# Optimization experiments

Hardware: AMD Instinct MI355X
Metric: run time of the kernel (lower is better)

Reference implementation:

```python
import jax, jax.numpy as jnp
import numpy as np

N = 25600            # 64 graphs x 400 ROIs
F_IN = 400
H = 128
E = 512000           # 8000 edges per graph
B = 64
G = 8
OUT = 2
NPG = 400            # nodes per graph
EPG = E // B         # edges per graph
BN_EPS = 1e-5


def _xavier(k, shape):
    lim = float(np.sqrt(6.0 / (shape[0] + shape[1])))
    return jax.random.uniform(k, shape, jnp.float32, -lim, lim)


def setup_inputs() -> dict:
    key = jax.random.key(0)
    ks = jax.random.split(key, 16)
    inp = {}
    inp["x"] = jax.random.normal(ks[0], (N, F_IN), jnp.float32)
    # within-graph random edges: local index + graph offset
    src_l = jax.random.randint(ks[1], (E,), 0, NPG, jnp.int32)
    dst_l = jax.random.randint(ks[2], (E,), 0, NPG, jnp.int32)
    off = (jnp.arange(E, dtype=jnp.int32) // EPG) * NPG
    inp["edge_index"] = jnp.stack([src_l + off, dst_l + off])
    inp["batch"] = (jnp.arange(N, dtype=jnp.int32) // NPG)
    inp["group_ids"] = jax.random.randint(ks[3], (N,), 0, G, jnp.int32)
    inp["ge"] = _xavier(ks[4], (G, 2))
    inp["he"] = _xavier(ks[5], (2, 2))
    dims = [(F_IN + 4, H), (H, H), (H, H)]
    for i, (di, do) in enumerate(dims):
        k1, k2 = jax.random.split(ks[6 + i])
        inp[f"w{i}a"] = _xavier(k1, (di, do))
        inp[f"b{i}a"] = jnp.zeros((do,), jnp.float32)
        inp[f"g{i}"] = jnp.ones((do,), jnp.float32)
        inp[f"be{i}"] = jnp.zeros((do,), jnp.float32)
        inp[f"w{i}b"] = _xavier(k2, (do, do))
        inp[f"b{i}b"] = jnp.zeros((do,), jnp.float32)
    inp["wfa"] = _xavier(ks[10], (H, H))
    inp["bfa"] = jnp.zeros((H,), jnp.float32)
    inp["wfb"] = _xavier(ks[11], (H, OUT))
    inp["bfb"] = jnp.zeros((OUT,), jnp.float32)
    return inp


def _bn(h, gamma, beta):
    # BatchNorm1d in training mode: stats over node dimension
    mu = jnp.mean(h, axis=0, keepdims=True)
    var = jnp.var(h, axis=0, keepdims=True)
    return gamma * (h - mu) * jax.lax.rsqrt(var + BN_EPS) + beta


def reference(x, edge_index, batch, group_ids, ge, he,
              w0a, b0a, g0, be0, w0b, b0b,
              w1a, b1a, g1, be1, w1b, b1b,
              w2a, b2a, g2, be2, w2b, b2b,
              wfa, bfa, wfb, bfb):
    n = x.shape[0]
    hemi = jnp.arange(n) % 2                      # [1::2] = 1
    h = jnp.concatenate([x, ge[group_ids], he[hemi]], axis=-1)  # [N, F_IN+4]
    src, dst = edge_index[0], edge_index[1]
    layers = [(w0a, b0a, g0, be0, w0b, b0b),
              (w1a, b1a, g1, be1, w1b, b1b),
              (w2a, b2a, g2, be2, w2b, b2b)]
    for wa, ba, g, be, wb, bb in layers:
        # GINConv (eps=0): x_i + sum_{(j,i)} x_j, then 2-layer MLP w/ batchnorm
        agg = jax.ops.segment_sum(h[src], dst, num_segments=N)
        z = h + agg
        z = jax.nn.relu(_bn(z @ wa + ba, g, be))  # dropout = identity (eval)
        h = jax.nn.relu(z @ wb + bb)              # outer ReLU from forward()
    pooled = jax.ops.segment_sum(h, batch, num_segments=B)  # global_add_pool
    return jax.nn.relu(pooled @ wfa + bfa) @ wfb + bfb
```

## Files before the change

kernel.cpp:

```cpp
#include <hip/hip_runtime.h>

#define N_NODES 25600
#define F_IN 400
#define NE 512000
#define NB 64
#define NPG 400
#define EPG 8000
#define BN_EPS 1e-5f

#define S_ROWS 448
#define S_COLS 448
#define S_COLS2 (S_COLS / 2)
#define AGG_TILES 7
#define SB_RPB 112
#define K0PAD 448

typedef __attribute__((ext_vector_type(8))) short short8;
typedef __attribute__((ext_vector_type(4))) short short4_t;
typedef __attribute__((ext_vector_type(4))) float floatx4;

__device__ __forceinline__ unsigned short f2bf(float f) {
    unsigned int u = __float_as_uint(f);
    u += 0x7FFF + ((u >> 16) & 1);
    return (unsigned short)(u >> 16);
}
__device__ __forceinline__ float bf2f(unsigned short s) {
    return __uint_as_float((unsigned int)s << 16);
}
__device__ __forceinline__ short u8bf(unsigned v) {
    return (short)(__float_as_uint((float)v) >> 16);
}


__global__ __launch_bounds__(256) void prep(const int* __restrict__ src,
                                            const int* __restrict__ dst,
                                            unsigned char* __restrict__ Sb,
                                            const float* __restrict__ wa0, const float* __restrict__ wa1,
                                            const float* __restrict__ wa2, const float* __restrict__ wb0,
                                            const float* __restrict__ wb1, const float* __restrict__ wb2,
                                            unsigned short* __restrict__ t0, unsigned short* __restrict__ t1,
                                            unsigned short* __restrict__ t2, unsigned short* __restrict__ t3,
                                            unsigned short* __restrict__ t4, unsigned short* __restrict__ t5,
                                            float* __restrict__ pstat) {
    __shared__ int cnt32[SB_RPB * NPG / 4];
    int tid = threadIdx.x;
    if (blockIdx.x < 256) {
        int b = blockIdx.x;
        int g = b >> 2, part = b & 3;
        int r0 = part * SB_RPB;
        for (int i = tid; i < SB_RPB * NPG / 4; i += 256) cnt32[i] = 0;
        __syncthreads();
        int ebase = g * EPG, nbase = g * NPG;
        for (int e = tid; e < EPG; e += 256) {
            int d = dst[ebase + e] - nbase;
            int dr = d - r0;
            if ((unsigned)dr < (unsigned)SB_RPB) {
                int s = src[ebase + e] - nbase;
                int idx = dr * NPG + s;
                atomicAdd(&cnt32[idx >> 2], (int)(1u << ((idx & 3) * 8)));
            }
        }
        __syncthreads();
        const unsigned char* cb = (const unsigned char*)cnt32;
        for (int i = tid; i < SB_RPB * (S_COLS / 8); i += 256) {
            int rr = i / (S_COLS / 8), c8 = (i % (S_COLS / 8)) * 8;
            int R = r0 + rr;
            unsigned pk = 0;
#pragma unroll
            for (int j = 0; j < 8; ++j) {
                int c = c8 + j;
                unsigned v = 0;
                if (R < NPG && c < NPG) v = (unsigned)cb[rr * NPG + c] + (c == R ? 1u : 0u);
                pk |= (v & 15u) << (4 * j);
            }
            *(unsigned*)&Sb[((size_t)g * S_ROWS + R) * S_COLS2 + (c8 >> 1)] = pk;
        }
        return;
    }
    int idx = (blockIdx.x - 256) * 256 + tid;
    if (idx < 3 * 2048 + 8192) pstat[idx] = 0.f;
    if (idx < 128 * K0PAD) {
        int n = idx / K0PAD, k = idx - n * K0PAD;
        t0[idx] = (k < 400) ? f2bf(wa0[(size_t)k * 128 + n]) : (unsigned short)0;
        return;
    }
    idx -= 128 * K0PAD;
    if (idx >= 5 * 128 * 128) return;
    int seg = idx >> 14;
    int r = idx & 16383;
    int n = r >> 7, k = r & 127;
    const float* srcs[5] = {wb0, wa1, wb1, wa2, wb2};
    unsigned short* dsts[5] = {t3, t1, t4, t2, t5};
    dsts[seg][r] = f2bf(srcs[seg][(size_t)k * 128 + n]);
}


__global__ __launch_bounds__(256) void gemm_embed64(const float* __restrict__ A,
                                                    const unsigned short* __restrict__ Wt,
                                                    const float* __restrict__ Wfull,
                                                    const int* __restrict__ gid,
                                                    const float* __restrict__ ge,
                                                    const float* __restrict__ he,
                                                    unsigned short* __restrict__ CtT) {
    __shared__ __align__(16) unsigned short As[64][72];
    __shared__ __align__(16) unsigned short Bs[128][72];
    __shared__ float Wex[4][128];
    int tid = threadIdx.x;
    int m0 = blockIdx.x * 64;
    int wave = tid >> 6, lane = tid & 63;
    int wcol = wave * 32;
    int fm = lane & 15, quad = lane >> 4;

    for (int i = tid; i < 512; i += 256)
        Wex[i >> 7][i & 127] = Wfull[(size_t)(400 + (i >> 7)) * 128 + (i & 127)];

    floatx4 acc[4][2];
#pragma unroll
    for (int rt = 0; rt < 4; ++rt)
#pragma unroll
        for (int ct = 0; ct < 2; ++ct) acc[rt][ct] = (floatx4){0.f, 0.f, 0.f, 0.f};

    const int rA = tid >> 2, kcA = (tid & 3) * 16;
    const int nB = tid >> 1, kcB = (tid & 1) * 32;
    float4 aP0, aP1, aP2, aP3;
    short8 bP0, bP1, bP2, bP3;

    auto loadK = [&](int ks) {
        int k0 = ks * 64;
        int kg = k0 + kcA;
        const float* ar = A + (size_t)(m0 + rA) * F_IN;
        if (kg + 15 < 400) {
            aP0 = *(const float4*)(ar + kg);
            aP1 = *(const float4*)(ar + kg + 4);
            aP2 = *(const float4*)(ar + kg + 8);
            aP3 = *(const float4*)(ar + kg + 12);
        } else {
            float v[16];
#pragma unroll
            for (int j = 0; j < 16; ++j) v[j] = (kg + j < 400) ? ar[kg + j] : 0.f;
            aP0 = (float4){v[0], v[1], v[2], v[3]};
            aP1 = (float4){v[4], v[5], v[6], v[7]};
            aP2 = (float4){v[8], v[9], v[10], v[11]};
            aP3 = (float4){v[12], v[13], v[14], v[15]};
        }
        const unsigned short* wr = Wt + (size_t)nB * K0PAD + k0 + kcB;
        bP0 = *(const short8*)wr;
        bP1 = *(const short8*)(wr + 8);
        bP2 = *(const short8*)(wr + 16);
        bP3 = *(const short8*)(wr + 24);
    };

    loadK(0);
    for (int ks = 0; ks < 7; ++ks) {
        {
            short8 s0, s1;
            s0[0] = (short)f2bf(aP0.x); s0[1] = (short)f2bf(aP0.y);
            s0[2] = (short)f2bf(aP0.z); s0[3] = (short)f2bf(aP0.w);
            s0[4] = (short)f2bf(aP1.x); s0[5] = (short)f2bf(aP1.y);
            s0[6] = (short)f2bf(aP1.z); s0[7] = (short)f2bf(aP1.w);
            s1[0] = (short)f2bf(aP2.x); s1[1] = (short)f2bf(aP2.y);
            s1[2] = (short)f2bf(aP2.z); s1[3] = (short)f2bf(aP2.w);
            s1[4] = (short)f2bf(aP3.x); s1[5] = (short)f2bf(aP3.y);
            s1[6] = (short)f2bf(aP3.z); s1[7] = (short)f2bf(aP3.w);
            *(short8*)&As[rA][kcA] = s0;
            *(short8*)&As[rA][kcA + 8] = s1;
            *(short8*)&Bs[nB][kcB] = bP0;
            *(short8*)&Bs[nB][kcB + 8] = bP1;
            *(short8*)&Bs[nB][kcB + 16] = bP2;
            *(short8*)&Bs[nB][kcB + 24] = bP3;
        }
        __syncthreads();
        if (ks + 1 < 7) loadK(ks + 1);
#pragma unroll
        for (int k0l = 0; k0l < 64; k0l += 32) {
            short8 af[4], bf[2];
#pragma unroll
            for (int rt = 0; rt < 4; ++rt)
                af[rt] = *(const short8*)&As[rt * 16 + fm][k0l + quad * 8];
#pragma unroll
            for (int ct = 0; ct < 2; ++ct)
                bf[ct] = *(const short8*)&Bs[wcol + ct * 16 + fm][k0l + quad * 8];
#pragma unroll
            for (int rt = 0; rt < 4; ++rt)
#pragma unroll
                for (int ct = 0; ct < 2; ++ct)
                    acc[rt][ct] = __builtin_amdgcn_mfma_f32_16x16x32_bf16(
                        af[rt], bf[ct], acc[rt][ct], 0, 0, 0);
        }
        __syncthreads();
    }

#pragma unroll
    for (int rt = 0; rt < 4; ++rt) {
#pragma unroll
        for (int ct = 0; ct < 2; ++ct) {
            int col = wcol + ct * 16 + fm;
            int row0 = m0 + rt * 16 + quad * 4;
            ushort4 o;
#pragma unroll
            for (int r = 0; r < 4; ++r) {
                int row = row0 + r;
                int gv = gid[row];
                float v = acc[rt][ct][r]
                        + ge[gv * 2] * Wex[0][col] + ge[gv * 2 + 1] * Wex[1][col]
                        + he[(row & 1) * 2] * Wex[2][col] + he[(row & 1) * 2 + 1] * Wex[3][col];
                ((unsigned short*)&o)[r] = f2bf(v);
            }
            *(ushort4*)&CtT[(size_t)col * N_NODES + row0] = o;
        }
    }
}


__global__ __launch_bounds__(256) void agg_mfma(const unsigned char* __restrict__ Sb,
                                                const unsigned short* __restrict__ tT,
                                                const float* __restrict__ bias,
                                                unsigned short* __restrict__ z,
                                                float* __restrict__ psumG,
                                                float* __restrict__ psqG) {
    __shared__ __align__(16) unsigned short As[64][72];
    __shared__ __align__(16) unsigned short Bs[128][72];
    __shared__ float sw[4][2][16], qw[4][2][16];
    int tid = threadIdx.x;
    int b = blockIdx.x;
    int g = b & 63;
    int tile = b >> 6;
    int m0l = tile * 64;
    int node0 = g * NPG;
    int wave = tid >> 6, lane = tid & 63;
    int wcol = wave * 32;
    int fm = lane & 15, quad = lane >> 4;

    floatx4 acc[4][2];
#pragma unroll
    for (int rt = 0; rt < 4; ++rt)
#pragma unroll
        for (int ct = 0; ct < 2; ++ct) acc[rt][ct] = (floatx4){0.f, 0.f, 0.f, 0.f};

    const int rA = tid >> 2, kcA = (tid & 3) * 16;
    const int nB = tid >> 1, kcB = (tid & 1) * 32;
    unsigned long long aP;
    short8 bP0, bP1, bP2, bP3;

    auto loadK = [&](int ks) {
        int k0 = ks * 64;
        aP = *(const unsigned long long*)(Sb + ((size_t)g * S_ROWS + m0l + rA) * S_COLS2 + ((k0 + kcA) >> 1));
        const unsigned short* p = tT + (size_t)nB * N_NODES + node0 + k0 + kcB;
        bP0 = *(const short8*)p;
        bP1 = *(const short8*)(p + 8);
        bP2 = *(const short8*)(p + 16);
        bP3 = *(const short8*)(p + 24);
    };

    loadK(0);
    for (int ks = 0; ks < S_COLS / 64; ++ks) {
        {
            short8 s0, s1;
#pragma unroll
            for (int j = 0; j < 8; ++j) s0[j] = u8bf((unsigned)(aP >> (4 * j)) & 15u);
#pragma unroll
            for (int j = 0; j < 8; ++j) s1[j] = u8bf((unsigned)(aP >> (32 + 4 * j)) & 15u);
            *(short8*)&As[rA][kcA] = s0;
            *(short8*)&As[rA][kcA + 8] = s1;
            *(short8*)&Bs[nB][kcB] = bP0;
            *(short8*)&Bs[nB][kcB + 8] = bP1;
            *(short8*)&Bs[nB][kcB + 16] = bP2;
            *(short8*)&Bs[nB][kcB + 24] = bP3;
        }
        __syncthreads();
        if (ks + 1 < S_COLS / 64) loadK(ks + 1);
#pragma unroll
        for (int k0l = 0; k0l < 64; k0l += 32) {
            short8 af[4], bf[2];
#pragma unroll
            for (int rt = 0; rt < 4; ++rt)
                af[rt] = *(const short8*)&As[rt * 16 + fm][k0l + quad * 8];
#pragma unroll
            for (int ct = 0; ct < 2; ++ct)
                bf[ct] = *(const short8*)&Bs[wcol + ct * 16 + fm][k0l + quad * 8];
#pragma unroll
            for (int rt = 0; rt < 4; ++rt)
#pragma unroll
                for (int ct = 0; ct < 2; ++ct)
                    acc[rt][ct] = __builtin_amdgcn_mfma_f32_16x16x32_bf16(
                        af[rt], bf[ct], acc[rt][ct], 0, 0, 0);
        }
        __syncthreads();
    }

    {
        float scol[2] = {0.f, 0.f}, qcol[2] = {0.f, 0.f};
#pragma unroll
        for (int rt = 0; rt < 4; ++rt) {
#pragma unroll
            for (int ct = 0; ct < 2; ++ct) {
                int col = wcol + ct * 16 + fm;
                float bv = bias[col];
                int rbase = m0l + rt * 16 + quad * 4;
#pragma unroll
                for (int r = 0; r < 4; ++r) {
                    int rloc = rbase + r;
                    if (rloc < NPG) {
                        float v = acc[rt][ct][r] + bv;
                        z[(size_t)(node0 + rloc) * 128 + col] = f2bf(v);
                        scol[ct] += v;
                        qcol[ct] += v * v;
                    }
                }
            }
        }
#pragma unroll
        for (int ct = 0; ct < 2; ++ct) {
            scol[ct] += __shfl_xor(scol[ct], 16);
            scol[ct] += __shfl_xor(scol[ct], 32);
            qcol[ct] += __shfl_xor(qcol[ct], 16);
            qcol[ct] += __shfl_xor(qcol[ct], 32);
        }
        if (lane < 16) {
#pragma unroll
            for (int ct = 0; ct < 2; ++ct) { sw[wave][ct][lane] = scol[ct]; qw[wave][ct][lane] = qcol[ct]; }
        }
    }
    __syncthreads();
    if (tid < 128) {
        int c = tid;
        int wv = c >> 5, ct = (c >> 4) & 1, f = c & 15;
        int bucket = b & 7;
        atomicAdd(&psumG[bucket * 128 + c], sw[wv][ct][f]);
        atomicAdd(&psqG[bucket * 128 + c], qw[wv][ct][f]);
    }
}


#define MODE_FUSED 0
#define MODE_FINAL 1

template <int MODE>
__global__ __launch_bounds__(256) void gemm_post64(const unsigned short* __restrict__ z,
                                                   const float* __restrict__ psumG,
                                                   const float* __restrict__ psqG,
                                                   const float* __restrict__ gamma,
                                                   const float* __restrict__ beta,
                                                   const unsigned short* __restrict__ wtb,
                                                   const float* __restrict__ bb,
                                                   const unsigned short* __restrict__ wta_next,
                                                   unsigned short* __restrict__ CtT,
                                                   float* __restrict__ pooled) {
    __shared__ __align__(16) unsigned short Bs[128][72];
    __shared__ __align__(16) unsigned short hs[64][136];
    __shared__ float coefs[256];
    int tid = threadIdx.x;
    int m0 = blockIdx.x * 64;
    int wave = tid >> 6, lane = tid & 63;
    int wcol = wave * 32;
    int fm = lane & 15, quad = lane >> 4;

    if (tid < 128) {
        float S = 0.f, Q = 0.f;
#pragma unroll
        for (int b = 0; b < 8; ++b) { S += psumG[b * 128 + tid]; Q += psqG[b * 128 + tid]; }
        float invn = 1.0f / (float)N_NODES;
        float mu = S * invn;
        float var = Q * invn - mu * mu;
        float a = gamma[tid] * rsqrtf(var + BN_EPS);
        coefs[tid] = a;
        coefs[128 + tid] = beta[tid] - a * mu;
    }
    __syncthreads();

    floatx4 acc[4][2];
#pragma unroll
    for (int rt = 0; rt < 4; ++rt)
#pragma unroll
        for (int ct = 0; ct < 2; ++ct) acc[rt][ct] = (floatx4){0.f, 0.f, 0.f, 0.f};

    const int rA = tid >> 2, kcA = (tid & 3) * 16;
    const int nB = tid >> 1, kcB = (tid & 1) * 32;
    short8 aPa, aPb;
    short8 bP0, bP1, bP2, bP3;

    auto loadK1 = [&](int ks) {
        int k0 = ks * 64;
        const unsigned short* zr = &z[(size_t)(m0 + rA) * 128 + k0 + kcA];
        aPa = *(const short8*)zr;
        aPb = *(const short8*)(zr + 8);
        const unsigned short* wr = wtb + (size_t)nB * 128 + k0 + kcB;
        bP0 = *(const short8*)wr;
        bP1 = *(const short8*)(wr + 8);
        bP2 = *(const short8*)(wr + 16);
        bP3 = *(const short8*)(wr + 24);
    };

    loadK1(0);
    for (int ks = 0; ks < 2; ++ks) {
        {
            int kg = ks * 64 + kcA;
            short8 s0, s1;
#pragma unroll
            for (int j = 0; j < 8; ++j) {
                float v = fmaxf(coefs[kg + j] * bf2f((unsigned short)aPa[j]) + coefs[128 + kg + j], 0.f);
                s0[j] = (short)f2bf(v);
            }
#pragma unroll
            for (int j = 0; j < 8; ++j) {
                float v = fmaxf(coefs[kg + 8 + j] * bf2f((unsigned short)aPb[j]) + coefs[128 + kg + 8 + j], 0.f);
                s1[j] = (short)f2bf(v);
            }
            *(short8*)&hs[rA][kcA] = s0;
            *(short8*)&hs[rA][kcA + 8] = s1;
            *(short8*)&Bs[nB][kcB] = bP0;
            *(short8*)&Bs[nB][kcB + 8] = bP1;
            *(short8*)&Bs[nB][kcB + 16] = bP2;
            *(short8*)&Bs[nB][kcB + 24] = bP3;
        }
        __syncthreads();
        if (ks + 1 < 2) loadK1(ks + 1);
#pragma unroll
        for (int k0l = 0; k0l < 64; k0l += 32) {
            short8 af[4], bf[2];
#pragma unroll
            for (int rt = 0; rt < 4; ++rt)
                af[rt] = *(const short8*)&hs[rt * 16 + fm][k0l + quad * 8];
#pragma unroll
            for (int ct = 0; ct < 2; ++ct)
                bf[ct] = *(const short8*)&Bs[wcol + ct * 16 + fm][k0l + quad * 8];
#pragma unroll
            for (int rt = 0; rt < 4; ++rt)
#pragma unroll
                for (int ct = 0; ct < 2; ++ct)
                    acc[rt][ct] = __builtin_amdgcn_mfma_f32_16x16x32_bf16(
                        af[rt], bf[ct], acc[rt][ct], 0, 0, 0);
        }
        __syncthreads();
    }

    if (MODE == MODE_FINAL) {
        float rsum[4][2];
#pragma unroll
        for (int rt = 0; rt < 4; ++rt)
#pragma unroll
            for (int ct = 0; ct < 2; ++ct) {
                int col = wcol + ct * 16 + fm;
                float bv = bb[col];
                float s = 0.f;
#pragma unroll
                for (int r = 0; r < 4; ++r) s += fmaxf(acc[rt][ct][r] + bv, 0.f);
                rsum[rt][ct] = s;
            }
        bool uniform = (m0 / NPG) == ((m0 + 63) / NPG);
        if (uniform) {
            int gph = m0 / NPG;
#pragma unroll
            for (int ct = 0; ct < 2; ++ct) {
                float cs = rsum[0][ct] + rsum[1][ct] + rsum[2][ct] + rsum[3][ct];
                cs += __shfl_xor(cs, 16);
                cs += __shfl_xor(cs, 32);
                if (lane < 16) atomicAdd(&pooled[gph * 128 + wcol + ct * 16 + fm], cs);
            }
        } else {
#pragma unroll
            for (int rt = 0; rt < 4; ++rt)
#pragma unroll
                for (int ct = 0; ct < 2; ++ct) {
                    int gph = (m0 + rt * 16 + quad * 4) / NPG;
                    atomicAdd(&pooled[gph * 128 + wcol + ct * 16 + fm], rsum[rt][ct]);
                }
        }
        return;
    }

#pragma unroll
    for (int rt = 0; rt < 4; ++rt)
#pragma unroll
        for (int ct = 0; ct < 2; ++ct) {
            int col = wcol + ct * 16 + fm;
            float bv = bb[col];
            int rbase = rt * 16 + quad * 4;
#pragma unroll
            for (int r = 0; r < 4; ++r)
                hs[rbase + r][col] = f2bf(fmaxf(acc[rt][ct][r] + bv, 0.f));
        }
    __syncthreads();

#pragma unroll
    for (int rt = 0; rt < 4; ++rt)
#pragma unroll
        for (int ct = 0; ct < 2; ++ct) acc[rt][ct] = (floatx4){0.f, 0.f, 0.f, 0.f};

    const int kcB2 = (tid & 1) * 16;
    for (int ks = 0; ks < 4; ++ks) {
        int k0 = ks * 32;
        {
            const unsigned short* wr = wta_next + (size_t)nB * 128 + k0 + kcB2;
            *(short8*)&Bs[nB][kcB2] = *(const short8*)wr;
            *(short8*)&Bs[nB][kcB2 + 8] = *(const short8*)(wr + 8);
        }
        __syncthreads();
        {
            short8 af[4], bf[2];
#pragma unroll
            for (int rt = 0; rt < 4; ++rt)
                af[rt] = *(const short8*)&hs[rt * 16 + fm][k0 + quad * 8];
#pragma unroll
            for (int ct = 0; ct < 2; ++ct)
                bf[ct] = *(const short8*)&Bs[wcol + ct * 16 + fm][quad * 8];
#pragma unroll
            for (int rt = 0; rt < 4; ++rt)
#pragma unroll
                for (int ct = 0; ct < 2; ++ct)
                    acc[rt][ct] = __builtin_amdgcn_mfma_f32_16x16x32_bf16(
                        af[rt], bf[ct], acc[rt][ct], 0, 0, 0);
        }
        __syncthreads();
    }

#pragma unroll
    for (int rt = 0; rt < 4; ++rt)
#pragma unroll
        for (int ct = 0; ct < 2; ++ct) {
            int col = wcol + ct * 16 + fm;
            int row0 = m0 + rt * 16 + quad * 4;
            ushort4 o;
#pragma unroll
            for (int r = 0; r < 4; ++r) ((unsigned short*)&o)[r] = f2bf(acc[rt][ct][r]);
            *(ushort4*)&CtT[(size_t)col * N_NODES + row0] = o;
        }
}


__global__ __launch_bounds__(128) void head(const float* __restrict__ pooled,
                                            const float* __restrict__ wfa,
                                            const float* __restrict__ bfa,
                                            const float* __restrict__ wfb,
                                            const float* __restrict__ bfb,
                                            float* __restrict__ out) {
    int g = blockIdx.x;
    int f = threadIdx.x;
    __shared__ float pl[128];
    pl[f] = pooled[g * 128 + f];
    __syncthreads();
    float a = bfa[f];
    for (int k = 0; k < 128; ++k) a += pl[k] * wfa[k * 128 + f];
    float p2 = fmaxf(a, 0.f);
    __shared__ float o0[128], o1[128];
    o0[f] = p2 * wfb[f * 2 + 0];
    o1[f] = p2 * wfb[f * 2 + 1];
    __syncthreads();
    if (f == 0) {
        float a0 = bfb[0], a1 = bfb[1];
#pragma unroll
        for (int k = 0; k < 128; ++k) { a0 += o0[k]; a1 += o1[k]; }
        out[g * 2 + 0] = a0;
        out[g * 2 + 1] = a1;
    }
}


extern "C" void kernel_launch(void* const* d_in, const int* in_sizes, int n_in,
                              void* d_out, int out_size, void* d_ws, size_t ws_size,
                              hipStream_t stream) {
    const float* x   = (const float*)d_in[0];
    const int* ei    = (const int*)d_in[1];
    const int* gid   = (const int*)d_in[3];
    const float* ge  = (const float*)d_in[4];
    const float* he  = (const float*)d_in[5];
    const float* wa[3] = {(const float*)d_in[6],  (const float*)d_in[12], (const float*)d_in[18]};
    const float* ba[3] = {(const float*)d_in[7],  (const float*)d_in[13], (const float*)d_in[19]};
    const float* gg[3] = {(const float*)d_in[8],  (const float*)d_in[14], (const float*)d_in[20]};
    const float* bb_[3]= {(const float*)d_in[9],  (const float*)d_in[15], (const float*)d_in[21]};
    const float* wb[3] = {(const float*)d_in[10], (const float*)d_in[16], (const float*)d_in[22]};
    const float* bbias[3] = {(const float*)d_in[11], (const float*)d_in[17], (const float*)d_in[23]};
    const float* wfa = (const float*)d_in[24];
    const float* bfa = (const float*)d_in[25];
    const float* wfb = (const float*)d_in[26];
    const float* bfb = (const float*)d_in[27];
    float* out = (float*)d_out;

    char* ws = (char*)d_ws;
    size_t o = 0;
    auto alloc = [&](size_t bytes) { char* p = ws + o; o += (bytes + 255) & ~(size_t)255; return p; };
    unsigned short* tT = (unsigned short*)alloc((size_t)128 * N_NODES * 2 + 1024);
    unsigned short* z  = (unsigned short*)alloc((size_t)N_NODES * 128 * 2);
    unsigned char* Sb  = (unsigned char*)alloc((size_t)NB * S_ROWS * S_COLS2);
    float* pstat = (float*)alloc((3 * 2048 + 8192) * 4);
    unsigned short* wt0  = (unsigned short*)alloc(128 * K0PAD * 2);
    unsigned short* wta1 = (unsigned short*)alloc(128 * 128 * 2);
    unsigned short* wta2 = (unsigned short*)alloc(128 * 128 * 2);
    unsigned short* wtb0 = (unsigned short*)alloc(128 * 128 * 2);
    unsigned short* wtb1 = (unsigned short*)alloc(128 * 128 * 2);
    unsigned short* wtb2 = (unsigned short*)alloc(128 * 128 * 2);
    (void)ws_size; (void)in_sizes; (void)n_in; (void)out_size;

    const int* esrc_in = ei;
    const int* edst_in = ei + NE;

    prep<<<256 + 544, 256, 0, stream>>>(esrc_in, edst_in, Sb,
                                        wa[0], wa[1], wa[2], wb[0], wb[1], wb[2],
                                        wt0, wta1, wta2, wtb0, wtb1, wtb2, pstat);

    float* ps0 = pstat;            float* pq0 = pstat + 1024;
    float* ps1 = pstat + 2048;     float* pq1 = pstat + 3072;
    float* ps2 = pstat + 4096;     float* pq2 = pstat + 5120;
    float* pooled = pstat + 6144;

    gemm_embed64<<<400, 256, 0, stream>>>(x, wt0, wa[0], gid, ge, he, tT);
    agg_mfma<<<NB * AGG_TILES, 256, 0, stream>>>(Sb, tT, ba[0], z, ps0, pq0);
    gemm_post64<MODE_FUSED><<<400, 256, 0, stream>>>(z, ps0, pq0, gg[0], bb_[0],
                                                     wtb0, bbias[0], wta1, tT, nullptr);
    agg_mfma<<<NB * AGG_TILES, 256, 0, stream>>>(Sb, tT, ba[1], z, ps1, pq1);
    gemm_post64<MODE_FUSED><<<400, 256, 0, stream>>>(z, ps1, pq1, gg[1], bb_[1],
                                                     wtb1, bbias[1], wta2, tT, nullptr);
    agg_mfma<<<NB * AGG_TILES, 256, 0, stream>>>(Sb, tT, ba[2], z, ps2, pq2);
    gemm_post64<MODE_FINAL><<<400, 256, 0, stream>>>(z, ps2, pq2, gg[2], bb_[2],
                                                     wtb2, bbias[2], nullptr, nullptr, pooled);

    head<<<NB, 128, 0, stream>>>(pooled, wfa, bfa, wfb, bfb, out);
}
```

Measured before the change: 254.1 us.

## Fuse GIN layers and head into persistent per-graph kernel with grid barriers

Replaces the seven per-layer kernel launches (aggregation, post-GEMM, head) with one persistent kernel of 64 blocks of 1024 threads, one block per graph. Layers are separated by atomic-counter grid barriers, which are needed for the global batchnorm statistics, and pooling plus the MLP head run inside the same kernel. This removes launch overhead and inter-kernel gaps, but only 64 blocks occupy the GPU, so most CUs sit idle and parallelism drops. The barrier also assumes all 64 blocks are co-resident.

```diff
diff --git a/kernel.cpp b/kernel.cpp
--- a/kernel.cpp
+++ b/kernel.cpp
@@ -11,13 +11,13 @@
 #define S_ROWS 448
 #define S_COLS 448
 #define S_COLS2 (S_COLS / 2)
-#define AGG_TILES 7
 #define SB_RPB 112
 #define K0PAD 448
 
 typedef __attribute__((ext_vector_type(8))) short short8;
-typedef __attribute__((ext_vector_type(4))) short short4_t;
 typedef __attribute__((ext_vector_type(4))) float floatx4;
+typedef unsigned short us;
+typedef unsigned long long u64;
 
 __device__ __forceinline__ unsigned short f2bf(float f) {
     unsigned int u = __float_as_uint(f);
@@ -38,10 +38,10 @@
                                             const float* __restrict__ wa0, const float* __restrict__ wa1,
                                             const float* __restrict__ wa2, const float* __restrict__ wb0,
                                             const float* __restrict__ wb1, const float* __restrict__ wb2,
-                                            unsigned short* __restrict__ t0, unsigned short* __restrict__ t1,
-                                            unsigned short* __restrict__ t2, unsigned short* __restrict__ t3,
-                                            unsigned short* __restrict__ t4, unsigned short* __restrict__ t5,
-                                            float* __restrict__ pstat) {
+                                            us* __restrict__ t0, us* __restrict__ t1,
+                                            us* __restrict__ t2, us* __restrict__ t3,
+                                            us* __restrict__ t4, us* __restrict__ t5,
+                                            float* __restrict__ pstat, us* __restrict__ tTz) {
     __shared__ int cnt32[SB_RPB * NPG / 4];
     int tid = threadIdx.x;
     if (blockIdx.x < 256) {
@@ -79,6 +79,7 @@
     }
     int idx = (blockIdx.x - 256) * 256 + tid;
     if (idx < 3 * 2048 + 8192) pstat[idx] = 0.f;
+    if (idx < 512) tTz[(size_t)128 * N_NODES + idx] = 0;
     if (idx < 128 * K0PAD) {
         int n = idx / K0PAD, k = idx - n * K0PAD;
         t0[idx] = (k < 400) ? f2bf(wa0[(size_t)k * 128 + n]) : (unsigned short)0;
@@ -90,20 +91,20 @@
     int r = idx & 16383;
     int n = r >> 7, k = r & 127;
     const float* srcs[5] = {wb0, wa1, wb1, wa2, wb2};
-    unsigned short* dsts[5] = {t3, t1, t4, t2, t5};
+    us* dsts[5] = {t3, t1, t4, t2, t5};
     dsts[seg][r] = f2bf(srcs[seg][(size_t)k * 128 + n]);
 }
 
 
 __global__ __launch_bounds__(256) void gemm_embed64(const float* __restrict__ A,
-                                                    const unsigned short* __restrict__ Wt,
+                                                    const us* __restrict__ Wt,
                                                     const float* __restrict__ Wfull,
                                                     const int* __restrict__ gid,
                                                     const float* __restrict__ ge,
                                                     const float* __restrict__ he,
-                                                    unsigned short* __restrict__ CtT) {
-    __shared__ __align__(16) unsigned short As[64][72];
-    __shared__ __align__(16) unsigned short Bs[128][72];
+                                                    us* __restrict__ CtT) {
+    __shared__ __align__(16) us As[64][72];
+    __shared__ __align__(16) us Bs[128][72];
     __shared__ float Wex[4][128];
     int tid = threadIdx.x;
     int m0 = blockIdx.x * 64;
@@ -143,7 +144,7 @@
             aP2 = (float4){v[8], v[9], v[10], v[11]};
             aP3 = (float4){v[12], v[13], v[14], v[15]};
         }
-        const unsigned short* wr = Wt + (size_t)nB * K0PAD + k0 + kcB;
+        const us* wr = Wt + (size_t)nB * K0PAD + k0 + kcB;
         bP0 = *(const short8*)wr;
         bP1 = *(const short8*)(wr + 8);
         bP2 = *(const short8*)(wr + 16);
@@ -212,153 +213,150 @@
 }
 
 
-__global__ __launch_bounds__(256) void agg_mfma(const unsigned char* __restrict__ Sb,
-                                                const unsigned short* __restrict__ tT,
-                                                const float* __restrict__ bias,
-                                                unsigned short* __restrict__ z,
-                                                float* __restrict__ psumG,
-                                                float* __restrict__ psqG) {
-    __shared__ __align__(16) unsigned short As[64][72];
-    __shared__ __align__(16) unsigned short Bs[128][72];
-    __shared__ float sw[4][2][16], qw[4][2][16];
-    int tid = threadIdx.x;
-    int b = blockIdx.x;
-    int g = b & 63;
-    int tile = b >> 6;
-    int m0l = tile * 64;
+
+__device__ __forceinline__ void gbar(unsigned* bar, unsigned tgt) {
+    __syncthreads();
+    if (threadIdx.x == 0) {
+        __hip_atomic_fetch_add(bar, 1u, __ATOMIC_RELAXED, __HIP_MEMORY_SCOPE_AGENT);
+        while (__hip_atomic_load(bar, __ATOMIC_RELAXED, __HIP_MEMORY_SCOPE_AGENT) < tgt)
+            __builtin_amdgcn_s_sleep(8);
+        asm volatile("" ::: "memory");
+    }
+    __syncthreads();
+}
+
+__device__ __forceinline__ void p_agg(unsigned char* smem, int g, int tid,
+        const unsigned char* __restrict__ Sb, const us* __restrict__ tT,
+        const float* __restrict__ ba, us* __restrict__ zg,
+        float* __restrict__ psum, float* __restrict__ psq, int bucket) {
+    us (*As)[72] = (us(*)[72])smem;
+    us (*Bs)[72] = (us(*)[72])(smem + 36864);
+    float (*rs)[4][2][16] = (float(*)[4][2][16])(smem + 55296);
+    float (*rq)[4][2][16] = (float(*)[4][2][16])(smem + 57344);
+    int wave = tid >> 6, lane = tid & 63;
+    int wrow = wave >> 2, wc4 = wave & 3;
+    int wcol = wc4 * 32;
+    int fm = lane & 15, quad = lane >> 4;
     int node0 = g * NPG;
-    int wave = tid >> 6, lane = tid & 63;
-    int wcol = wave * 32;
-    int fm = lane & 15, quad = lane >> 4;
-
-    floatx4 acc[4][2];
-#pragma unroll
-    for (int rt = 0; rt < 4; ++rt)
-#pragma unroll
-        for (int ct = 0; ct < 2; ++ct) acc[rt][ct] = (floatx4){0.f, 0.f, 0.f, 0.f};
-
     const int rA = tid >> 2, kcA = (tid & 3) * 16;
-    const int nB = tid >> 1, kcB = (tid & 1) * 32;
-    unsigned long long aP;
-    short8 bP0, bP1, bP2, bP3;
-
-    auto loadK = [&](int ks) {
-        int k0 = ks * 64;
-        aP = *(const unsigned long long*)(Sb + ((size_t)g * S_ROWS + m0l + rA) * S_COLS2 + ((k0 + kcA) >> 1));
-        const unsigned short* p = tT + (size_t)nB * N_NODES + node0 + k0 + kcB;
-        bP0 = *(const short8*)p;
-        bP1 = *(const short8*)(p + 8);
-        bP2 = *(const short8*)(p + 16);
-        bP3 = *(const short8*)(p + 24);
-    };
-
-    loadK(0);
-    for (int ks = 0; ks < S_COLS / 64; ++ks) {
-        {
-            short8 s0, s1;
-#pragma unroll
-            for (int j = 0; j < 8; ++j) s0[j] = u8bf((unsigned)(aP >> (4 * j)) & 15u);
-#pragma unroll
-            for (int j = 0; j < 8; ++j) s1[j] = u8bf((unsigned)(aP >> (32 + 4 * j)) & 15u);
-            *(short8*)&As[rA][kcA] = s0;
-            *(short8*)&As[rA][kcA + 8] = s1;
-            *(short8*)&Bs[nB][kcB] = bP0;
-            *(short8*)&Bs[nB][kcB + 8] = bP1;
-            *(short8*)&Bs[nB][kcB + 16] = bP2;
-            *(short8*)&Bs[nB][kcB + 24] = bP3;
-        }
-        __syncthreads();
-        if (ks + 1 < S_COLS / 64) loadK(ks + 1);
-#pragma unroll
-        for (int k0l = 0; k0l < 64; k0l += 32) {
-            short8 af[4], bf[2];
-#pragma unroll
-            for (int rt = 0; rt < 4; ++rt)
-                af[rt] = *(const short8*)&As[rt * 16 + fm][k0l + quad * 8];
-#pragma unroll
-            for (int ct = 0; ct < 2; ++ct)
-                bf[ct] = *(const short8*)&Bs[wcol + ct * 16 + fm][k0l + quad * 8];
-#pragma unroll
-            for (int rt = 0; rt < 4; ++rt)
+    const int nB = tid >> 3, kcB = (tid & 7) * 8;
+    float scol[2] = {0.f, 0.f}, qcol[2] = {0.f, 0.f};
+
+    for (int R0 = 0; R0 < 400; R0 += 256) {
+        floatx4 acc[4][2];
+#pragma unroll
+        for (int rt = 0; rt < 4; ++rt)
+#pragma unroll
+            for (int ct = 0; ct < 2; ++ct) acc[rt][ct] = (floatx4){0.f, 0.f, 0.f, 0.f};
+
+        u64 aP;
+        short8 bP;
+        auto loadK = [&](int ks) {
+            int row = R0 + rA;
+            aP = (row < S_ROWS)
+               ? *(const u64*)(Sb + ((size_t)g * S_ROWS + row) * S_COLS2 + ks * 32 + (tid & 3) * 8)
+               : 0ull;
+            bP = *(const short8*)(tT + (size_t)nB * N_NODES + node0 + ks * 64 + kcB);
+        };
+
+        loadK(0);
+        for (int ks = 0; ks < 7; ++ks) {
+            {
+                short8 s0, s1;
+#pragma unroll
+                for (int j = 0; j < 8; ++j) s0[j] = u8bf((unsigned)(aP >> (4 * j)) & 15u);
+#pragma unroll
+                for (int j = 0; j < 8; ++j) s1[j] = u8bf((unsigned)(aP >> (32 + 4 * j)) & 15u);
+                *(short8*)&As[rA][kcA] = s0;
+                *(short8*)&As[rA][kcA + 8] = s1;
+                *(short8*)&Bs[nB][kcB] = bP;
+            }
+            __syncthreads();
+            if (ks + 1 < 7) loadK(ks + 1);
+#pragma unroll
+            for (int k0l = 0; k0l < 64; k0l += 32) {
+                short8 af[4], bf[2];
+#pragma unroll
+                for (int rt = 0; rt < 4; ++rt)
+                    af[rt] = *(const short8*)&As[wrow * 64 + rt * 16 + fm][k0l + quad * 8];
 #pragma unroll
                 for (int ct = 0; ct < 2; ++ct)
-                    acc[rt][ct] = __builtin_amdgcn_mfma_f32_16x16x32_bf16(
-                        af[rt], bf[ct], acc[rt][ct], 0, 0, 0);
-        }
-        __syncthreads();
-    }
-
-    {
-        float scol[2] = {0.f, 0.f}, qcol[2] = {0.f, 0.f};
+                    bf[ct] = *(const short8*)&Bs[wcol + ct * 16 + fm][k0l + quad * 8];
+#pragma unroll
+                for (int rt = 0; rt < 4; ++rt)
+#pragma unroll
+                    for (int ct = 0; ct < 2; ++ct)
+                        acc[rt][ct] = __builtin_amdgcn_mfma_f32_16x16x32_bf16(
+                            af[rt], bf[ct], acc[rt][ct], 0, 0, 0);
+            }
+            __syncthreads();
+        }
+
 #pragma unroll
         for (int rt = 0; rt < 4; ++rt) {
 #pragma unroll
             for (int ct = 0; ct < 2; ++ct) {
                 int col = wcol + ct * 16 + fm;
-                float bv = bias[col];
-                int rbase = m0l + rt * 16 + quad * 4;
-#pragma unroll
-                for (int r = 0; r < 4; ++r) {
-                    int rloc = rbase + r;
-                    if (rloc < NPG) {
+                float bv = ba[col];
+                int rbase = R0 + wrow * 64 + rt * 16 + quad * 4;
+                if (rbase < 400) {
+#pragma unroll
+                    for (int r = 0; r < 4; ++r) {
                         float v = acc[rt][ct][r] + bv;
-                        z[(size_t)(node0 + rloc) * 128 + col] = f2bf(v);
+                        zg[(size_t)(rbase + r) * 128 + col] = f2bf(v);
                         scol[ct] += v;
                         qcol[ct] += v * v;
                     }
                 }
             }
         }
-#pragma unroll
-        for (int ct = 0; ct < 2; ++ct) {
-            scol[ct] += __shfl_xor(scol[ct], 16);
-            scol[ct] += __shfl_xor(scol[ct], 32);
-            qcol[ct] += __shfl_xor(qcol[ct], 16);
-            qcol[ct] += __shfl_xor(qcol[ct], 32);
-        }
-        if (lane < 16) {
-#pragma unroll
-            for (int ct = 0; ct < 2; ++ct) { sw[wave][ct][lane] = scol[ct]; qw[wave][ct][lane] = qcol[ct]; }
-        }
+    }
+
+#pragma unroll
+    for (int ct = 0; ct < 2; ++ct) {
+        scol[ct] += __shfl_xor(scol[ct], 16);
+        scol[ct] += __shfl_xor(scol[ct], 32);
+        qcol[ct] += __shfl_xor(qcol[ct], 16);
+        qcol[ct] += __shfl_xor(qcol[ct], 32);
+    }
+    if (lane < 16) {
+#pragma unroll
+        for (int ct = 0; ct < 2; ++ct) { rs[wrow][wc4][ct][lane] = scol[ct]; rq[wrow][wc4][ct][lane] = qcol[ct]; }
     }
     __syncthreads();
     if (tid < 128) {
-        int c = tid;
-        int wv = c >> 5, ct = (c >> 4) & 1, f = c & 15;
-        int bucket = b & 7;
-        atomicAdd(&psumG[bucket * 128 + c], sw[wv][ct][f]);
-        atomicAdd(&psqG[bucket * 128 + c], qw[wv][ct][f]);
-    }
-}
-
-
-#define MODE_FUSED 0
-#define MODE_FINAL 1
-
-template <int MODE>
-__global__ __launch_bounds__(256) void gemm_post64(const unsigned short* __restrict__ z,
-                                                   const float* __restrict__ psumG,
-                                                   const float* __restrict__ psqG,
-                                                   const float* __restrict__ gamma,
-                                                   const float* __restrict__ beta,
-                                                   const unsigned short* __restrict__ wtb,
-                                                   const float* __restrict__ bb,
-                                                   const unsigned short* __restrict__ wta_next,
-                                                   unsigned short* __restrict__ CtT,
-                                                   float* __restrict__ pooled) {
-    __shared__ __align__(16) unsigned short Bs[128][72];
-    __shared__ __align__(16) unsigned short hs[64][136];
-    __shared__ float coefs[256];
-    int tid = threadIdx.x;
-    int m0 = blockIdx.x * 64;
+        int wc = tid >> 5, ct = (tid >> 4) & 1, f = tid & 15;
+        float S = 0.f, Q = 0.f;
+#pragma unroll
+        for (int wr = 0; wr < 4; ++wr) { S += rs[wr][wc][ct][f]; Q += rq[wr][wc][ct][f]; }
+        atomicAdd(&psum[bucket * 128 + tid], S);
+        atomicAdd(&psq[bucket * 128 + tid], Q);
+    }
+}
+
+template <int FINAL>
+__device__ __forceinline__ void p_post(unsigned char* smem, int g, int tid,
+        const us* __restrict__ zg, const float* __restrict__ psum, const float* __restrict__ psq,
+        const float* __restrict__ gamma, const float* __restrict__ beta,
+        const us* __restrict__ wtb, const float* __restrict__ bb,
+        const us* __restrict__ wta_next, us* __restrict__ tT,
+        float& pool0, float& pool1) {
+    us (*hs)[136] = (us(*)[136])smem;
+    us (*Bs)[72]  = (us(*)[72])(smem + 34816);
+    float* coefs  = (float*)(smem + 53248);
     int wave = tid >> 6, lane = tid & 63;
-    int wcol = wave * 32;
+    int wrow = wave >> 2;
+    int wcol = (wave & 3) * 32;
     int fm = lane & 15, quad = lane >> 4;
+    int node0 = g * NPG;
 
     if (tid < 128) {
         float S = 0.f, Q = 0.f;
 #pragma unroll
-        for (int b = 0; b < 8; ++b) { S += psumG[b * 128 + tid]; Q += psqG[b * 128 + tid]; }
+        for (int b = 0; b < 8; ++b) {
+            S += __hip_atomic_load(&psum[b * 128 + tid], __ATOMIC_RELAXED, __HIP_MEMORY_SCOPE_AGENT);
+            Q += __hip_atomic_load(&psq[b * 128 + tid], __ATOMIC_RELAXED, __HIP_MEMORY_SCOPE_AGENT);
+        }
         float invn = 1.0f / (float)N_NODES;
         float mu = S * invn;
         float var = Q * invn - mu * mu;
@@ -368,185 +366,195 @@
     }
     __syncthreads();
 
-    floatx4 acc[4][2];
-#pragma unroll
-    for (int rt = 0; rt < 4; ++rt)
-#pragma unroll
-        for (int ct = 0; ct < 2; ++ct) acc[rt][ct] = (floatx4){0.f, 0.f, 0.f, 0.f};
-
-    const int rA = tid >> 2, kcA = (tid & 3) * 16;
-    const int nB = tid >> 1, kcB = (tid & 1) * 32;
-    short8 aPa, aPb;
-    short8 bP0, bP1, bP2, bP3;
-
-    auto loadK1 = [&](int ks) {
-        int k0 = ks * 64;
-        const unsigned short* zr = &z[(size_t)(m0 + rA) * 128 + k0 + kcA];
-        aPa = *(const short8*)zr;
-        aPb = *(const short8*)(zr + 8);
-        const unsigned short* wr = wtb + (size_t)nB * 128 + k0 + kcB;
-        bP0 = *(const short8*)wr;
-        bP1 = *(const short8*)(wr + 8);
-        bP2 = *(const short8*)(wr + 16);
-        bP3 = *(const short8*)(wr + 24);
-    };
-
-    loadK1(0);
-    for (int ks = 0; ks < 2; ++ks) {
-        {
-            int kg = ks * 64 + kcA;
-            short8 s0, s1;
-#pragma unroll
-            for (int j = 0; j < 8; ++j) {
-                float v = fmaxf(coefs[kg + j] * bf2f((unsigned short)aPa[j]) + coefs[128 + kg + j], 0.f);
-                s0[j] = (short)f2bf(v);
-            }
-#pragma unroll
-            for (int j = 0; j < 8; ++j) {
-                float v = fmaxf(coefs[kg + 8 + j] * bf2f((unsigned short)aPb[j]) + coefs[128 + kg + 8 + j], 0.f);
-                s1[j] = (short)f2bf(v);
-            }
-            *(short8*)&hs[rA][kcA] = s0;
-            *(short8*)&hs[rA][kcA + 8] = s1;
-            *(short8*)&Bs[nB][kcB] = bP0;
-            *(short8*)&Bs[nB][kcB + 8] = bP1;
-            *(short8*)&Bs[nB][kcB + 16] = bP2;
-            *(short8*)&Bs[nB][kcB + 24] = bP3;
-        }
-        __syncthreads();
-        if (ks + 1 < 2) loadK1(ks + 1);
-#pragma unroll
-        for (int k0l = 0; k0l < 64; k0l += 32) {
-            short8 af[4], bf[2];
-#pragma unroll
-            for (int rt = 0; rt < 4; ++rt)
-                af[rt] = *(const short8*)&hs[rt * 16 + fm][k0l + quad * 8];
-#pragma unroll
-            for (int ct = 0; ct < 2; ++ct)
-                bf[ct] = *(const short8*)&Bs[wcol + ct * 16 + fm][k0l + quad * 8];
-#pragma unroll
-            for (int rt = 0; rt < 4; ++rt)
+    const int rA = tid >> 3, kcA = (tid & 7) * 8;
+    const int nB = tid >> 3, kcB = (tid & 7) * 8;
+
+    for (int R0 = 0; R0 < 400; R0 += 128) {
+        floatx4 acc[2][2];
+#pragma unroll
+        for (int rt = 0; rt < 2; ++rt)
+#pragma unroll
+            for (int ct = 0; ct < 2; ++ct) acc[rt][ct] = (floatx4){0.f, 0.f, 0.f, 0.f};
+
+        short8 aP, bP;
+        auto loadK1 = [&](int ks) {
+            int row = R0 + rA;
+            if (row < 400) aP = *(const short8*)(zg + (size_t)row * 128 + ks * 64 + kcA);
+            else { short8 zz = {0,0,0,0,0,0,0,0}; aP = zz; }
+            bP = *(const short8*)(wtb + (size_t)nB * 128 + ks * 64 + kcB);
+        };
+
+        loadK1(0);
+        for (int ks = 0; ks < 2; ++ks) {
+            {
+                int kg = ks * 64 + kcA;
+                short8 s0;
+#pragma unroll
+                for (int j = 0; j < 8; ++j) {
+                    float v = fmaxf(coefs[kg + j] * bf2f((unsigned short)aP[j]) + coefs[128 + kg + j], 0.f);
+                    s0[j] = (short)f2bf(v);
+                }
+                *(short8*)&hs[rA][kcA] = s0;
+                *(short8*)&Bs[nB][kcB] = bP;
+            }
+            __syncthreads();
+            if (ks + 1 < 2) loadK1(ks + 1);
+#pragma unroll
+            for (int k0l = 0; k0l < 64; k0l += 32) {
+                short8 af[2], bf[2];
+#pragma unroll
+                for (int rt = 0; rt < 2; ++rt)
+                    af[rt] = *(const short8*)&hs[wrow * 32 + rt * 16 + fm][k0l + quad * 8];
 #pragma unroll
                 for (int ct = 0; ct < 2; ++ct)
-                    acc[rt][ct] = __builtin_amdgcn_mfma_f32_16x16x32_bf16(
-                        af[rt], bf[ct], acc[rt][ct], 0, 0, 0);
-        }
-        __syncthreads();
-    }
-
-    if (MODE == MODE_FINAL) {
-        float rsum[4][2];
-#pragma unroll
-        for (int rt = 0; rt < 4; ++rt)
+                    bf[ct] = *(const short8*)&Bs[wcol + ct * 16 + fm][k0l + quad * 8];
+#pragma unroll
+                for (int rt = 0; rt < 2; ++rt)
+#pragma unroll
+                    for (int ct = 0; ct < 2; ++ct)
+                        acc[rt][ct] = __builtin_amdgcn_mfma_f32_16x16x32_bf16(
+                            af[rt], bf[ct], acc[rt][ct], 0, 0, 0);
+            }
+            __syncthreads();
+        }
+
+        if (FINAL) {
+#pragma unroll
+            for (int rt = 0; rt < 2; ++rt)
+#pragma unroll
+                for (int ct = 0; ct < 2; ++ct) {
+                    int col = wcol + ct * 16 + fm;
+                    float bv = bb[col];
+                    int rbase = R0 + wrow * 32 + rt * 16 + quad * 4;
+                    if (rbase < 400) {
+                        float s = 0.f;
+#pragma unroll
+                        for (int r = 0; r < 4; ++r) s += fmaxf(acc[rt][ct][r] + bv, 0.f);
+                        if (ct == 0) pool0 += s; else pool1 += s;
+                    }
+                }
+            continue;
+        }
+
+#pragma unroll
+        for (int rt = 0; rt < 2; ++rt)
 #pragma unroll
             for (int ct = 0; ct < 2; ++ct) {
                 int col = wcol + ct * 16 + fm;
                 float bv = bb[col];
-                float s = 0.f;
-#pragma unroll
-                for (int r = 0; r < 4; ++r) s += fmaxf(acc[rt][ct][r] + bv, 0.f);
-                rsum[rt][ct] = s;
-            }
-        bool uniform = (m0 / NPG) == ((m0 + 63) / NPG);
-        if (uniform) {
-            int gph = m0 / NPG;
+                int rbase = wrow * 32 + rt * 16 + quad * 4;
+#pragma unroll
+                for (int r = 0; r < 4; ++r)
+                    hs[rbase + r][col] = f2bf(fmaxf(acc[rt][ct][r] + bv, 0.f));
+            }
+        __syncthreads();
+
+#pragma unroll
+        for (int rt = 0; rt < 2; ++rt)
+#pragma unroll
+            for (int ct = 0; ct < 2; ++ct) acc[rt][ct] = (floatx4){0.f, 0.f, 0.f, 0.f};
+
+        for (int ks = 0; ks < 2; ++ks) {
+            *(short8*)&Bs[nB][kcB] = *(const short8*)(wta_next + (size_t)nB * 128 + ks * 64 + kcB);
+            __syncthreads();
+#pragma unroll
+            for (int k0l = 0; k0l < 64; k0l += 32) {
+                short8 af[2], bf[2];
+#pragma unroll
+                for (int rt = 0; rt < 2; ++rt)
+                    af[rt] = *(const short8*)&hs[wrow * 32 + rt * 16 + fm][ks * 64 + k0l + quad * 8];
+#pragma unroll
+                for (int ct = 0; ct < 2; ++ct)
+                    bf[ct] = *(const short8*)&Bs[wcol + ct * 16 + fm][k0l + quad * 8];
+#pragma unroll
+                for (int rt = 0; rt < 2; ++rt)
+#pragma unroll
+                    for (int ct = 0; ct < 2; ++ct)
+                        acc[rt][ct] = __builtin_amdgcn_mfma_f32_16x16x32_bf16(
+                            af[rt], bf[ct], acc[rt][ct], 0, 0, 0);
+            }
+            __syncthreads();
+        }
+
+#pragma unroll
+        for (int rt = 0; rt < 2; ++rt)
 #pragma unroll
             for (int ct = 0; ct < 2; ++ct) {
-                float cs = rsum[0][ct] + rsum[1][ct] + rsum[2][ct] + rsum[3][ct];
-                cs += __shfl_xor(cs, 16);
-                cs += __shfl_xor(cs, 32);
-                if (lane < 16) atomicAdd(&pooled[gph * 128 + wcol + ct * 16 + fm], cs);
-            }
-        } else {
-#pragma unroll
-            for (int rt = 0; rt < 4; ++rt)
-#pragma unroll
-                for (int ct = 0; ct < 2; ++ct) {
-                    int gph = (m0 + rt * 16 + quad * 4) / NPG;
-                    atomicAdd(&pooled[gph * 128 + wcol + ct * 16 + fm], rsum[rt][ct]);
+                int col = wcol + ct * 16 + fm;
+                int row0 = R0 + wrow * 32 + rt * 16 + quad * 4;
+                if (row0 < 400) {
+                    ushort4 o;
+#pragma unroll
+                    for (int r = 0; r < 4; ++r) ((unsigned short*)&o)[r] = f2bf(acc[rt][ct][r]);
+                    *(ushort4*)&tT[(size_t)col * N_NODES + node0 + row0] = o;
                 }
-        }
-        return;
-    }
-
-#pragma unroll
-    for (int rt = 0; rt < 4; ++rt)
-#pragma unroll
-        for (int ct = 0; ct < 2; ++ct) {
-            int col = wcol + ct * 16 + fm;
-            float bv = bb[col];
-            int rbase = rt * 16 + quad * 4;
-#pragma unroll
-            for (int r = 0; r < 4; ++r)
-                hs[rbase + r][col] = f2bf(fmaxf(acc[rt][ct][r] + bv, 0.f));
-        }
-    __syncthreads();
-
-#pragma unroll
-    for (int rt = 0; rt < 4; ++rt)
-#pragma unroll
-        for (int ct = 0; ct < 2; ++ct) acc[rt][ct] = (floatx4){0.f, 0.f, 0.f, 0.f};
-
-    const int kcB2 = (tid & 1) * 16;
-    for (int ks = 0; ks < 4; ++ks) {
-        int k0 = ks * 32;
-        {
-            const unsigned short* wr = wta_next + (size_t)nB * 128 + k0 + kcB2;
-            *(short8*)&Bs[nB][kcB2] = *(const short8*)wr;
-            *(short8*)&Bs[nB][kcB2 + 8] = *(const short8*)(wr + 8);
-        }
+            }
         __syncthreads();
-        {
-            short8 af[4], bf[2];
-#pragma unroll
-            for (int rt = 0; rt < 4; ++rt)
-                af[rt] = *(const short8*)&hs[rt * 16 + fm][k0 + quad * 8];
-#pragma unroll
-            for (int ct = 0; ct < 2; ++ct)
-                bf[ct] = *(const short8*)&Bs[wcol + ct * 16 + fm][quad * 8];
-#pragma unroll
-            for (int rt = 0; rt < 4; ++rt)
-#pragma unroll
-                for (int ct = 0; ct < 2; ++ct)
-                    acc[rt][ct] = __builtin_amdgcn_mfma_f32_16x16x32_bf16(
-                        af[rt], bf[ct], acc[rt][ct], 0, 0, 0);
-        }
-        __syncthreads();
-    }
-
-#pragma unroll
-    for (int rt = 0; rt < 4; ++rt)
-#pragma unroll
-        for (int ct = 0; ct < 2; ++ct) {
-            int col = wcol + ct * 16 + fm;
-            int row0 = m0 + rt * 16 + quad * 4;
-            ushort4 o;
-#pragma unroll
-            for (int r = 0; r < 4; ++r) ((unsigned short*)&o)[r] = f2bf(acc[rt][ct][r]);
-            *(ushort4*)&CtT[(size_t)col * N_NODES + row0] = o;
-        }
-}
-
-
-__global__ __launch_bounds__(128) void head(const float* __restrict__ pooled,
-                                            const float* __restrict__ wfa,
-                                            const float* __restrict__ bfa,
-                                            const float* __restrict__ wfb,
-                                            const float* __restrict__ bfb,
-                                            float* __restrict__ out) {
-    int g = blockIdx.x;
-    int f = threadIdx.x;
-    __shared__ float pl[128];
-    pl[f] = pooled[g * 128 + f];
-    __syncthreads();
-    float a = bfa[f];
-    for (int k = 0; k < 128; ++k) a += pl[k] * wfa[k * 128 + f];
-    float p2 = fmaxf(a, 0.f);
-    __shared__ float o0[128], o1[128];
-    o0[f] = p2 * wfb[f * 2 + 0];
-    o1[f] = p2 * wfb[f * 2 + 1];
-    __syncthreads();
-    if (f == 0) {
+    }
+}
+
+__global__ __launch_bounds__(1024, 4) void persist_gnn(
+        const unsigned char* __restrict__ Sb, us* __restrict__ tT, us* __restrict__ z,
+        float* __restrict__ pstat,
+        const us* __restrict__ wtb0, const us* __restrict__ wta1,
+        const us* __restrict__ wtb1, const us* __restrict__ wta2,
+        const us* __restrict__ wtb2,
+        const float* __restrict__ ba0, const float* __restrict__ ba1, const float* __restrict__ ba2,
+        const float* __restrict__ gg0, const float* __restrict__ be0, const float* __restrict__ bbias0,
+        const float* __restrict__ gg1, const float* __restrict__ be1, const float* __restrict__ bbias1,
+        const float* __restrict__ gg2, const float* __restrict__ be2, const float* __restrict__ bbias2,
+        const float* __restrict__ wfa, const float* __restrict__ bfa,
+        const float* __restrict__ wfb, const float* __restrict__ bfb,
+        unsigned* __restrict__ bar, float* __restrict__ out) {
+    __shared__ __align__(16) unsigned char smem[59392];
+    int g = blockIdx.x, tid = threadIdx.x;
+    int wave = tid >> 6, lane = tid & 63;
+    int wrow = wave >> 2, wc4 = wave & 3;
+    us* zg = z + (size_t)g * NPG * 128;
+    float pool0 = 0.f, pool1 = 0.f;
+
+    p_agg(smem, g, tid, Sb, tT, ba0, zg, pstat + 0, pstat + 1024, g & 7);
+    gbar(bar, 64);
+    p_post<0>(smem, g, tid, zg, pstat + 0, pstat + 1024, gg0, be0, wtb0, bbias0, wta1, tT, pool0, pool1);
+    __syncthreads();
+
+    p_agg(smem, g, tid, Sb, tT, ba1, zg, pstat + 2048, pstat + 3072, g & 7);
+    gbar(bar, 128);
+    p_post<0>(smem, g, tid, zg, pstat + 2048, pstat + 3072, gg1, be1, wtb1, bbias1, wta2, tT, pool0, pool1);
+    __syncthreads();
+
+    p_agg(smem, g, tid, Sb, tT, ba2, zg, pstat + 4096, pstat + 5120, g & 7);
+    gbar(bar, 192);
+    p_post<1>(smem, g, tid, zg, pstat + 4096, pstat + 5120, gg2, be2, wtb2, bbias2, nullptr, tT, pool0, pool1);
+    __syncthreads();
+
+    float* pl = (float*)smem;
+    float (*red)[4][2][16] = (float(*)[4][2][16])(smem + 512);
+    pool0 += __shfl_xor(pool0, 16); pool0 += __shfl_xor(pool0, 32);
+    pool1 += __shfl_xor(pool1, 16); pool1 += __shfl_xor(pool1, 32);
+    if (lane < 16) { red[wrow][wc4][0][lane] = pool0; red[wrow][wc4][1][lane] = pool1; }
+    __syncthreads();
+    if (tid < 128) {
+        int wc = tid >> 5, ct = (tid >> 4) & 1, f = tid & 15;
+        float s = 0.f;
+#pragma unroll
+        for (int wr = 0; wr < 4; ++wr) s += red[wr][wc][ct][f];
+        pl[tid] = s;
+    }
+    __syncthreads();
+
+    float* o0 = (float*)(smem + 512);
+    float* o1 = (float*)(smem + 1024);
+    if (tid < 128) {
+        int f = tid;
+        float a = bfa[f];
+        for (int k = 0; k < 128; ++k) a += pl[k] * wfa[k * 128 + f];
+        float p2 = fmaxf(a, 0.f);
+        o0[f] = p2 * wfb[f * 2 + 0];
+        o1[f] = p2 * wfb[f * 2 + 1];
+    }
+    __syncthreads();
+    if (tid == 0) {
         float a0 = bfb[0], a1 = bfb[1];
 #pragma unroll
         for (int k = 0; k < 128; ++k) { a0 += o0[k]; a1 += o1[k]; }
@@ -579,40 +587,33 @@
     char* ws = (char*)d_ws;
     size_t o = 0;
     auto alloc = [&](size_t bytes) { char* p = ws + o; o += (bytes + 255) & ~(size_t)255; return p; };
-    unsigned short* tT = (unsigned short*)alloc((size_t)128 * N_NODES * 2 + 1024);
-    unsigned short* z  = (unsigned short*)alloc((size_t)N_NODES * 128 * 2);
+    us* tT = (us*)alloc((size_t)128 * N_NODES * 2 + 1024);
+    us* z  = (us*)alloc((size_t)N_NODES * 128 * 2);
     unsigned char* Sb  = (unsigned char*)alloc((size_t)NB * S_ROWS * S_COLS2);
     float* pstat = (float*)alloc((3 * 2048 + 8192) * 4);
-    unsigned short* wt0  = (unsigned short*)alloc(128 * K0PAD * 2);
-    unsigned short* wta1 = (unsigned short*)alloc(128 * 128 * 2);
-    unsigned short* wta2 = (unsigned short*)alloc(128 * 128 * 2);
-    unsigned short* wtb0 = (unsigned short*)alloc(128 * 128 * 2);
-    unsigned short* wtb1 = (unsigned short*)alloc(128 * 128 * 2);
-    unsigned short* wtb2 = (unsigned short*)alloc(128 * 128 * 2);
+    us* wt0  = (us*)alloc(128 * K0PAD * 2);
+    us* wta1 = (us*)alloc(128 * 128 * 2);
+    us* wta2 = (us*)alloc(128 * 128 * 2);
+    us* wtb0 = (us*)alloc(128 * 128 * 2);
+    us* wtb1 = (us*)alloc(128 * 128 * 2);
+    us* wtb2 = (us*)alloc(128 * 128 * 2);
+    unsigned* bar = (unsigned*)alloc(256);
     (void)ws_size; (void)in_sizes; (void)n_in; (void)out_size;
 
-    const int* esrc_in = ei;
-    const int* edst_in = ei + NE;
-
-    prep<<<256 + 544, 256, 0, stream>>>(esrc_in, edst_in, Sb,
+    hipMemsetAsync(bar, 0, 256, stream);
+
+    prep<<<256 + 544, 256, 0, stream>>>(ei, ei + NE, Sb,
                                         wa[0], wa[1], wa[2], wb[0], wb[1], wb[2],
-                                        wt0, wta1, wta2, wtb0, wtb1, wtb2, pstat);
-
-    float* ps0 = pstat;            float* pq0 = pstat + 1024;
-    float* ps1 = pstat + 2048;     float* pq1 = pstat + 3072;
-    float* ps2 = pstat + 4096;     float* pq2 = pstat + 5120;
-    float* pooled = pstat + 6144;
+                                        wt0, wta1, wta2, wtb0, wtb1, wtb2, pstat, tT);
 
     gemm_embed64<<<400, 256, 0, stream>>>(x, wt0, wa[0], gid, ge, he, tT);
-    agg_mfma<<<NB * AGG_TILES, 256, 0, stream>>>(Sb, tT, ba[0], z, ps0, pq0);
-    gemm_post64<MODE_FUSED><<<400, 256, 0, stream>>>(z, ps0, pq0, gg[0], bb_[0],
-                                                     wtb0, bbias[0], wta1, tT, nullptr);
-    agg_mfma<<<NB * AGG_TILES, 256, 0, stream>>>(Sb, tT, ba[1], z, ps1, pq1);
-    gemm_post64<MODE_FUSED><<<400, 256, 0, stream>>>(z, ps1, pq1, gg[1], bb_[1],
-                                                     wtb1, bbias[1], wta2, tT, nullptr);
-    agg_mfma<<<NB * AGG_TILES, 256, 0, stream>>>(Sb, tT, ba[2], z, ps2, pq2);
-    gemm_post64<MODE_FINAL><<<400, 256, 0, stream>>>(z, ps2, pq2, gg[2], bb_[2],
-                                                     wtb2, bbias[2], nullptr, nullptr, pooled);
-
-    head<<<NB, 128, 0, stream>>>(pooled, wfa, bfa, wfb, bfb, out);
-}
+
+    persist_gnn<<<64, 1024, 0, stream>>>(Sb, tT, z, pstat,
+                                         wtb0, wta1, wtb1, wta2, wtb2,
+                                         ba[0], ba[1], ba[2],
+                                         gg[0], bb_[0], bbias[0],
+                                         gg[1], bb_[1], bbias[1],
+                                         gg[2], bb_[2], bbias[2],
+                                         wfa, bfa, wfb, bfb,
+                                         bar, out);
+}
```

Result: slower. 347.6 us (+36.8%).
